# Kernel tuning notes

Measured on AMD Instinct MI355X. Metric: run time of the kernel, lower is better.

The kernel has to match this reference:

```python
import jax, jax.numpy as jnp
import numpy as np

N_NODES = 100000
N_EDGES = 3200000
IN_DIM = 3
HID = 8
OUT_DIM = 1


def setup_inputs() -> dict:
    key = jax.random.key(0)
    ks = jax.random.split(key, 10)
    x = jax.random.normal(ks[0], (N_NODES, IN_DIM), dtype=jnp.float32)
    edge_index = jax.random.randint(ks[1], (2, N_EDGES), 0, N_NODES, dtype=jnp.int64)
    cat_dim = 2 * (HID + IN_DIM)  # 22
    s = lambda fan_in: 1.0 / np.sqrt(fan_in)
    W_in = jax.random.uniform(ks[2], (IN_DIM, HID), jnp.float32, -s(IN_DIM), s(IN_DIM))
    b_in = jnp.zeros((HID,), jnp.float32)
    W1 = jax.random.uniform(ks[3], (cat_dim, HID), jnp.float32, -s(cat_dim), s(cat_dim))
    b1 = jnp.zeros((HID,), jnp.float32)
    W2 = jax.random.uniform(ks[4], (HID, HID), jnp.float32, -s(HID), s(HID))
    b2 = jnp.zeros((HID,), jnp.float32)
    W_e = jax.random.uniform(ks[5], (cat_dim, OUT_DIM), jnp.float32, -s(cat_dim), s(cat_dim))
    b_e = jnp.zeros((OUT_DIM,), jnp.float32)
    return {"x": x, "edge_index": edge_index, "W_in": W_in, "b_in": b_in,
            "W1": W1, "b1": b1, "W2": W2, "b2": b2, "W_e": W_e, "b_e": b_e}


def reference(x, edge_index, W_in, b_in, W1, b1, W2, b2, W_e, b_e):
    src = edge_index[0]  # j (source)
    dst = edge_index[1]  # i (target)

    # inputnet: Linear + Tanh
    H = jnp.tanh(x @ W_in + b_in)               # [N, HID]
    feat = jnp.concatenate([H, x], axis=-1)      # [N, HID+IN_DIM]

    # One EdgeConv iteration (n_iters=1): message = nn(cat([x_i, x_j - x_i]))
    xi = feat[dst]                                # [E, 11]
    xj = feat[src]                                # [E, 11]
    e = jnp.concatenate([xi, xj - xi], axis=-1)   # [E, 22]
    m = jax.nn.sigmoid(e @ W1 + b1)               # [E, HID]
    m = jax.nn.sigmoid(m @ W2 + b2)               # [E, HID]
    H = jax.ops.segment_sum(m, dst, num_segments=N_NODES)  # scatter-add to targets
    feat = jnp.concatenate([H, x], axis=-1)       # [N, 11]

    # edgenetwork on concatenated endpoint features
    ef = jnp.concatenate([feat[src], feat[dst]], axis=-1)   # [E, 22]
    out = jax.nn.sigmoid(ef @ W_e + b_e)          # [E, 1]
    return out.squeeze(-1)                        # [E]
```

## Files before the change

kernel.cpp:

```cpp
#include <hip/hip_runtime.h>
#include <hip/hip_fp16.h>

#define TPB     256
#define BSH     9
#define BW      512
#define EPB     8192
#define NBMAX   256
#define S_SPLIT 16
#define FXS     2097152.0f
#define FXSI    (1.0f / 2097152.0f)

static __device__ __forceinline__ float sigmoidf(float v) {
    return __builtin_amdgcn_rcpf(1.0f + __expf(-v));
}

static __device__ __forceinline__ void unpack8(uint4 u, float o[8]) {
    union { unsigned int u; __half2 h; } c0, c1, c2, c3;
    c0.u = u.x; c1.u = u.y; c2.u = u.z; c3.u = u.w;
    float2 f0 = __half22float2(c0.h), f1 = __half22float2(c1.h);
    float2 f2 = __half22float2(c2.h), f3 = __half22float2(c3.h);
    o[0]=f0.x; o[1]=f0.y; o[2]=f1.x; o[3]=f1.y;
    o[4]=f2.x; o[5]=f2.y; o[6]=f3.x; o[7]=f3.y;
}

__global__ void k_prep(const float* __restrict__ x,
                       const float* __restrict__ W_in,
                       const float* __restrict__ b_in,
                       const float* __restrict__ W1,
                       const float* __restrict__ b1,
                       float* __restrict__ egi,
                       __half* __restrict__ egjh,
                       const int* __restrict__ dst,
                       int* __restrict__ raw,
                       int n_nodes, int n_edges, int NB, int NBLK) {
    __shared__ int cnt[NBMAX];
    int t = threadIdx.x;
    if ((int)blockIdx.x < NBLK) {
        for (int b = t; b < NB; b += TPB) cnt[b] = 0;
        __syncthreads();
        int e0 = blockIdx.x * EPB;
#pragma unroll
        for (int k = 0; k < EPB / (TPB * 4); ++k) {
            int e = e0 + k * TPB * 4 + t * 4;
            if (e + 3 < n_edges) {
                int4 d4 = *(const int4*)(dst + e);
                atomicAdd(&cnt[d4.x >> BSH], 1);
                atomicAdd(&cnt[d4.y >> BSH], 1);
                atomicAdd(&cnt[d4.z >> BSH], 1);
                atomicAdd(&cnt[d4.w >> BSH], 1);
            } else {
                int qe = min(e + 4, n_edges);
                for (int q = e; q < qe; ++q)
                    atomicAdd(&cnt[dst[q] >> BSH], 1);
            }
        }
        __syncthreads();
        for (int b = t; b < NB; b += TPB)
            raw[(size_t)blockIdx.x * NB + b] = cnt[b];
    } else {
        int n = ((int)blockIdx.x - NBLK) * TPB + t;
        if (n >= n_nodes) return;
        float x0 = x[3*n], x1 = x[3*n+1], x2 = x[3*n+2];
        float f[11];
#pragma unroll
        for (int c = 0; c < 8; ++c)
            f[c] = tanhf(b_in[c] + x0*W_in[c] + x1*W_in[8+c] + x2*W_in[16+c]);
        f[8] = x0; f[9] = x1; f[10] = x2;
        float giv[8], gjv[8];
#pragma unroll
        for (int h = 0; h < 8; ++h) {
            float vi = b1[h], vj = 0.0f;
#pragma unroll
            for (int k = 0; k < 11; ++k) {
                float wa = W1[k*8+h], wb = W1[(11+k)*8+h];
                vi += f[k] * (wa - wb);
                vj += f[k] * wb;
            }
            giv[h] = __expf(-vi); gjv[h] = __expf(-vj);
        }
        float4* gip = (float4*)(egi + (size_t)n * 8);
        gip[0] = make_float4(giv[0], giv[1], giv[2], giv[3]);
        gip[1] = make_float4(giv[4], giv[5], giv[6], giv[7]);
        __align__(16) __half hj[8];
#pragma unroll
        for (int k = 0; k < 8; ++k) hj[k] = __float2half_rn(gjv[k]);
        *(uint4*)(egjh + (size_t)n * 8) = *(const uint4*)hj;
    }
}

__global__ void k_scan_cols(const int* __restrict__ raw, int* __restrict__ rel,
                            int* __restrict__ totals, int NB, int NBLK) {
    __shared__ int s[TPB];
    int b = blockIdx.x, t = threadIdx.x;
    int carry = 0;
    for (int q = 0; q < NBLK; q += TPB) {
        int blk = q + t;
        int v = (blk < NBLK) ? raw[(size_t)blk * NB + b] : 0;
        __syncthreads();
        s[t] = v; __syncthreads();
        for (int o = 1; o < TPB; o <<= 1) {
            int u = (t >= o) ? s[t - o] : 0;
            __syncthreads();
            s[t] += u;
            __syncthreads();
        }
        if (blk < NBLK) rel[(size_t)blk * NB + b] = carry + s[t] - v;
        carry += s[TPB - 1];
    }
    if (t == 0) totals[b] = carry;
}

__global__ void k_base(const int* __restrict__ totals, int* __restrict__ base,
                       int NB) {
    __shared__ int s[NBMAX];
    int t = threadIdx.x;
    int v = (t < NB) ? ((totals[t] + 3) & ~3) : 0;
    s[t] = v; __syncthreads();
    for (int o = 1; o < NBMAX; o <<= 1) {
        int u = (t >= o) ? s[t - o] : 0;
        __syncthreads();
        s[t] += u;
        __syncthreads();
    }
    if (t < NB) base[t] = s[t] - v;
}

__launch_bounds__(TPB)
__global__ void k_scatter(const int* __restrict__ src, const int* __restrict__ dst,
                          const int* __restrict__ raw, const int* __restrict__ rel,
                          const int* __restrict__ base,
                          int* __restrict__ sorted, int n_edges, int NB) {
    __shared__ int stage[EPB];
    __shared__ int cnt[NBMAX];
    __shared__ int lscan[NBMAX];
    __shared__ int gd[NBMAX];
    __shared__ int s[TPB];
    int t = threadIdx.x;

    {
        int v = (t < NB) ? raw[(size_t)blockIdx.x * NB + t] : 0;
        s[t] = v; __syncthreads();
        for (int o = 1; o < TPB; o <<= 1) {
            int u = (t >= o) ? s[t - o] : 0;
            __syncthreads();
            s[t] += u;
            __syncthreads();
        }
        if (t < NB) {
            lscan[t] = s[t] - v;
            cnt[t]   = s[t] - v;
            gd[t]    = base[t] + rel[(size_t)blockIdx.x * NB + t];
        }
    }
    __syncthreads();

    int e0 = blockIdx.x * EPB;
#pragma unroll
    for (int k = 0; k < EPB / (TPB * 4); ++k) {
        int e = e0 + k * TPB * 4 + t * 4;
        if (e + 3 < n_edges) {
            int4 s4 = *(const int4*)(src + e);
            int4 d4 = *(const int4*)(dst + e);
            int p;
            p = atomicAdd(&cnt[d4.x >> BSH], 1); stage[p] = (s4.x << BSH) | (d4.x & (BW-1));
            p = atomicAdd(&cnt[d4.y >> BSH], 1); stage[p] = (s4.y << BSH) | (d4.y & (BW-1));
            p = atomicAdd(&cnt[d4.z >> BSH], 1); stage[p] = (s4.z << BSH) | (d4.z & (BW-1));
            p = atomicAdd(&cnt[d4.w >> BSH], 1); stage[p] = (s4.w << BSH) | (d4.w & (BW-1));
        } else {
            int qe = min(e + 4, n_edges);
            for (int q = e; q < qe; ++q) {
                int d = dst[q];
                int p = atomicAdd(&cnt[d >> BSH], 1);
                stage[p] = (src[q] << BSH) | (d & (BW - 1));
            }
        }
    }
    __syncthreads();

    int wid = t >> 6, lane = t & 63;
    for (int b = wid; b < NB; b += (TPB / 64)) {
        int ls = lscan[b];
        int le = cnt[b];
        int g0 = gd[b];
        for (int i = ls + lane; i < le; i += 64)
            sorted[g0 + (i - ls)] = stage[i];
    }
}

__launch_bounds__(TPB, 4)
__global__ void k_bucket(const int* __restrict__ sorted, const int* __restrict__ base,
                         const int* __restrict__ totals,
                         const float* __restrict__ egi, const __half* __restrict__ egjh,
                         const float* __restrict__ W2, const float* __restrict__ b2,
                         const float* __restrict__ W_e,
                         int* __restrict__ part, int n_nodes, int NB, int NBP) {
    __shared__ int sa[BW], sc[BW];
    int t = threadIdx.x;
    int sl = blockIdx.x / NBP;
    int b  = blockIdx.x - sl * NBP;
    if (b >= NB) return;

    int nb0 = b * BW;
    for (int i = t; i < BW; i += TPB) { sa[i] = 0; sc[i] = 0; }
    __syncthreads();

    int beg = base[b];
    int len = totals[b];
    int qs = (((len + S_SPLIT - 1) / S_SPLIT) + 3) & ~3;
    int s0 = beg + sl * qs;
    int s1 = min(beg + len, s0 + qs);

    for (int g = s0 + t * 4; g < s1; g += TPB * 4) {
        if (g + 4 <= s1) {
            int4 pp = *(const int4*)(sorted + g);
            int d[4]  = { pp.x & (BW-1), pp.y & (BW-1), pp.z & (BW-1), pp.w & (BW-1) };
            int sj[4] = { pp.x >> BSH,   pp.y >> BSH,   pp.z >> BSH,   pp.w >> BSH };
            float ej[4][8];
#pragma unroll
            for (int q = 0; q < 4; ++q)
                unpack8(*(const uint4*)(egjh + (size_t)sj[q] * 8), ej[q]);
            float m[4][8];
#pragma unroll
            for (int q = 0; q < 4; ++q) {
                const float4* ip = (const float4*)(egi + (size_t)(nb0 + d[q]) * 8);
                float4 A = ip[0], B = ip[1];
                float ei[8] = {A.x,A.y,A.z,A.w,B.x,B.y,B.z,B.w};
#pragma unroll
                for (int k = 0; k < 8; ++k)
                    m[q][k] = __builtin_amdgcn_rcpf(1.0f + ei[k] * ej[q][k]);
            }
            float pa[4] = {0,0,0,0}, pc[4] = {0,0,0,0};
#pragma unroll
            for (int h = 0; h < 8; ++h) {
                float bb = b2[h];
                float v[4] = {bb, bb, bb, bb};
#pragma unroll
                for (int k = 0; k < 8; ++k) {
                    float w = W2[k*8+h];
#pragma unroll
                    for (int q = 0; q < 4; ++q) v[q] += m[q][k] * w;
                }
                float wa = W_e[h], wc = W_e[11+h];
#pragma unroll
                for (int q = 0; q < 4; ++q) {
                    float z = sigmoidf(v[q]);
                    pa[q] += z * wa; pc[q] += z * wc;
                }
            }
#pragma unroll
            for (int q = 0; q < 4; ++q) {
                atomicAdd(&sa[d[q]], __float2int_rn(pa[q] * FXS));
                atomicAdd(&sc[d[q]], __float2int_rn(pc[q] * FXS));
            }
        } else {
            for (int e = g; e < s1; ++e) {
                int p = sorted[e];
                int dl = p & (BW - 1);
                float ej[8];
                unpack8(*(const uint4*)(egjh + (size_t)(p >> BSH) * 8), ej);
                const float4* ip = (const float4*)(egi + (size_t)(nb0 + dl) * 8);
                float4 A = ip[0], B = ip[1];
                float ei[8] = {A.x,A.y,A.z,A.w,B.x,B.y,B.z,B.w};
                float m[8];
#pragma unroll
                for (int k = 0; k < 8; ++k)
                    m[k] = __builtin_amdgcn_rcpf(1.0f + ei[k] * ej[k]);
                float pa = 0, pc = 0;
#pragma unroll
                for (int h = 0; h < 8; ++h) {
                    float v = b2[h];
#pragma unroll
                    for (int k = 0; k < 8; ++k) v += m[k] * W2[k*8+h];
                    float z = sigmoidf(v);
                    pa += z * W_e[h]; pc += z * W_e[11+h];
                }
                atomicAdd(&sa[dl], __float2int_rn(pa * FXS));
                atomicAdd(&sc[dl], __float2int_rn(pc * FXS));
            }
        }
    }
    __syncthreads();
    size_t row = (size_t)blockIdx.x * (2 * BW);
    for (int i = t; i < BW; i += TPB) {
        part[row + i]      = sa[i];
        part[row + BW + i] = sc[i];
    }
}

__global__ void k_acc(const int* __restrict__ part, const float* __restrict__ x,
                      const float* __restrict__ W_e, float* __restrict__ ac,
                      int n_nodes, int NBP) {
    int n = blockIdx.x * blockDim.x + threadIdx.x;
    if (n >= n_nodes) return;
    int b = n >> BSH, r = n & (BW - 1);
    int ia = 0, ic = 0;
#pragma unroll
    for (int s = 0; s < S_SPLIT; ++s) {
        const int* pp = part + ((size_t)(s * NBP + b)) * (2 * BW);
        ia += pp[r];
        ic += pp[BW + r];
    }
    float a = (float)ia * FXSI, c = (float)ic * FXSI;
    float x0 = x[3*n], x1 = x[3*n+1], x2 = x[3*n+2];
    a += x0 * W_e[8]  + x1 * W_e[9]  + x2 * W_e[10];
    c += x0 * W_e[19] + x1 * W_e[20] + x2 * W_e[21];
    ac[2*n]     = a;
    ac[2*n + 1] = c;
}

__global__ void k_out2(const int* __restrict__ src, const int* __restrict__ dst,
                       const float* __restrict__ ac, const float* __restrict__ b_e,
                       float* __restrict__ out, int n_edges) {
    float bb = b_e[0];
    int e = (blockIdx.x * blockDim.x + threadIdx.x) * 4;
    if (e + 3 < n_edges) {
        int4 s4 = *(const int4*)(src + e);
        int4 d4 = *(const int4*)(dst + e);
        float4 o;
        o.x = sigmoidf(ac[2*s4.x] + ac[2*d4.x + 1] + bb);
        o.y = sigmoidf(ac[2*s4.y] + ac[2*d4.y + 1] + bb);
        o.z = sigmoidf(ac[2*s4.z] + ac[2*d4.z + 1] + bb);
        o.w = sigmoidf(ac[2*s4.w] + ac[2*d4.w + 1] + bb);
        *(float4*)(out + e) = o;
    } else {
        for (int q = e; q < n_edges; ++q)
            out[q] = sigmoidf(ac[2*src[q]] + ac[2*dst[q] + 1] + bb);
    }
}

__global__ void k_nodes(const float* __restrict__ x, const float* __restrict__ W_in,
                        const float* __restrict__ b_in, float* __restrict__ feat,
                        float* __restrict__ H2, int n_nodes) {
    int i = blockIdx.x * blockDim.x + threadIdx.x;
    if (i >= n_nodes) return;
    float x0 = x[3*i], x1 = x[3*i+1], x2 = x[3*i+2];
    float h[8];
#pragma unroll
    for (int c = 0; c < 8; ++c)
        h[c] = tanhf(b_in[c] + x0*W_in[c] + x1*W_in[8+c] + x2*W_in[16+c]);
    float4* fp = (float4*)(feat + (size_t)i * 12);
    fp[0] = make_float4(h[0],h[1],h[2],h[3]);
    fp[1] = make_float4(h[4],h[5],h[6],h[7]);
    fp[2] = make_float4(x0,x1,x2,0.0f);
    float4* hp = (float4*)(H2 + (size_t)i * 8);
    hp[0] = make_float4(0,0,0,0); hp[1] = make_float4(0,0,0,0);
}

__global__ void k_edges(const int* __restrict__ src, const int* __restrict__ dst,
                        const float* __restrict__ feat, const float* __restrict__ W1,
                        const float* __restrict__ b1, const float* __restrict__ W2,
                        const float* __restrict__ b2, float* __restrict__ H2,
                        int n_edges) {
    __shared__ float sW1[176], sW2[64], sb1[8], sb2[8];
    for (int t = threadIdx.x; t < 176; t += blockDim.x) sW1[t] = W1[t];
    for (int t = threadIdx.x; t < 64;  t += blockDim.x) sW2[t] = W2[t];
    if (threadIdx.x < 8) { sb1[threadIdx.x]=b1[threadIdx.x]; sb2[threadIdx.x]=b2[threadIdx.x]; }
    __syncthreads();
    int e = blockIdx.x * blockDim.x + threadIdx.x;
    if (e >= n_edges) return;
    int j = src[e], i = dst[e];
    const float4* fi = (const float4*)(feat + (size_t)i * 12);
    const float4* fj = (const float4*)(feat + (size_t)j * 12);
    float4 i0=fi[0],i1=fi[1],i2=fi[2],j0=fj[0],j1=fj[1],j2=fj[2];
    float xi[11]={i0.x,i0.y,i0.z,i0.w,i1.x,i1.y,i1.z,i1.w,i2.x,i2.y,i2.z};
    float xj[11]={j0.x,j0.y,j0.z,j0.w,j1.x,j1.y,j1.z,j1.w,j2.x,j2.y,j2.z};
    float dd[11];
#pragma unroll
    for (int k = 0; k < 11; ++k) dd[k]=xj[k]-xi[k];
    float m[8];
#pragma unroll
    for (int h = 0; h < 8; ++h) {
        float v = sb1[h];
#pragma unroll
        for (int k = 0; k < 11; ++k) v += xi[k]*sW1[k*8+h];
#pragma unroll
        for (int k = 0; k < 11; ++k) v += dd[k]*sW1[(11+k)*8+h];
        m[h] = sigmoidf(v);
    }
    float m2[8];
#pragma unroll
    for (int h = 0; h < 8; ++h) {
        float v = sb2[h];
#pragma unroll
        for (int k = 0; k < 8; ++k) v += m[k]*sW2[k*8+h];
        m2[h] = sigmoidf(v);
    }
    float* hp = H2 + (size_t)i * 8;
#pragma unroll
    for (int h = 0; h < 8; ++h) atomicAdd(hp + h, m2[h]);
}

__global__ void k_out(const int* __restrict__ src, const int* __restrict__ dst,
                      const float* __restrict__ H2, const float* __restrict__ x,
                      const float* __restrict__ W_e, const float* __restrict__ b_e,
                      float* __restrict__ out, int n_edges) {
    __shared__ float sW[22]; __shared__ float sb;
    if (threadIdx.x < 22) sW[threadIdx.x] = W_e[threadIdx.x];
    if (threadIdx.x == 0) sb = b_e[0];
    __syncthreads();
    int e = blockIdx.x * blockDim.x + threadIdx.x;
    if (e >= n_edges) return;
    int j = src[e], i = dst[e];
    const float4* hj = (const float4*)(H2 + (size_t)j * 8);
    const float4* hi = (const float4*)(H2 + (size_t)i * 8);
    float4 a0=hj[0],a1=hj[1],c0=hi[0],c1=hi[1];
    float acc = sb;
    acc += a0.x*sW[0]+a0.y*sW[1]+a0.z*sW[2]+a0.w*sW[3];
    acc += a1.x*sW[4]+a1.y*sW[5]+a1.z*sW[6]+a1.w*sW[7];
    acc += x[3*(size_t)j]*sW[8]+x[3*(size_t)j+1]*sW[9]+x[3*(size_t)j+2]*sW[10];
    acc += c0.x*sW[11]+c0.y*sW[12]+c0.z*sW[13]+c0.w*sW[14];
    acc += c1.x*sW[15]+c1.y*sW[16]+c1.z*sW[17]+c1.w*sW[18];
    acc += x[3*(size_t)i]*sW[19]+x[3*(size_t)i+1]*sW[20]+x[3*(size_t)i+2]*sW[21];
    out[e] = sigmoidf(acc);
}

extern "C" void kernel_launch(void* const* d_in, const int* in_sizes, int n_in,
                              void* d_out, int out_size, void* d_ws, size_t ws_size,
                              hipStream_t stream) {
    const float* x    = (const float*)d_in[0];
    const int*   ei   = (const int*)d_in[1];
    const float* W_in = (const float*)d_in[2];
    const float* b_in = (const float*)d_in[3];
    const float* W1   = (const float*)d_in[4];
    const float* b1   = (const float*)d_in[5];
    const float* W2   = (const float*)d_in[6];
    const float* b2   = (const float*)d_in[7];
    const float* W_e  = (const float*)d_in[8];
    const float* b_e  = (const float*)d_in[9];

    const int n_nodes = in_sizes[0] / 3;
    const int n_edges = in_sizes[1] / 2;
    const int* src = ei;
    const int* dst = ei + n_edges;
    float* out = (float*)d_out;

    const int NB   = (n_nodes + BW - 1) >> BSH;
    const int NBP  = (NB + 7) & ~7;
    const int NBLK = (n_edges + EPB - 1) / EPB;
    const int NFB  = (n_nodes + TPB - 1) / TPB;

    size_t off = 0;
    auto carve = [&](size_t bytes) { size_t o = off; off += (bytes + 255) & ~(size_t)255; return o; };
    char* ws = (char*)d_ws;
    size_t o_egi    = carve((size_t)n_nodes * 8 * 4);
    size_t o_egjh   = carve((size_t)n_nodes * 8 * 2);
    size_t o_ac     = carve((size_t)n_nodes * 2 * 4);
    size_t o_raw    = carve((size_t)NBLK * NB * 4);
    size_t o_rel    = carve((size_t)NBLK * NB * 4);
    size_t o_totals = carve((size_t)NB * 4);
    size_t o_base   = carve(((size_t)NB + 1) * 4);
    size_t o_sorted = carve(((size_t)n_edges + 4 * NBMAX) * 4);
    size_t o_part   = carve((size_t)NBP * S_SPLIT * 2 * BW * 4);
    bool fast = (off <= ws_size) && (NB <= NBMAX);

    if (fast) {
        float*  egi    = (float*)(ws + o_egi);
        __half* egjh   = (__half*)(ws + o_egjh);
        float*  ac     = (float*)(ws + o_ac);
        int*    raw    = (int*)(ws + o_raw);
        int*    rel    = (int*)(ws + o_rel);
        int*    totals = (int*)(ws + o_totals);
        int*    base   = (int*)(ws + o_base);
        int*    sorted = (int*)(ws + o_sorted);
        int*    part   = (int*)(ws + o_part);

        k_prep     <<<NBLK + NFB, TPB, 0, stream>>>(x, W_in, b_in, W1, b1, egi, egjh,
                                                    dst, raw, n_nodes, n_edges, NB, NBLK);
        k_scan_cols<<<NB, TPB, 0, stream>>>(raw, rel, totals, NB, NBLK);
        k_base     <<<1, NBMAX, 0, stream>>>(totals, base, NB);
        k_scatter  <<<NBLK, TPB, 0, stream>>>(src, dst, raw, rel, base, sorted, n_edges, NB);
        k_bucket   <<<NBP * S_SPLIT, TPB, 0, stream>>>(sorted, base, totals, egi, egjh, W2, b2, W_e,
                                                       part, n_nodes, NB, NBP);
        k_acc      <<<(n_nodes + TPB - 1) / TPB, TPB, 0, stream>>>(part, x, W_e, ac, n_nodes, NBP);
        k_out2     <<<(n_edges / 4 + TPB - 1) / TPB + 1, TPB, 0, stream>>>(src, dst, ac, b_e, out, n_edges);
    } else {
        float* feat = (float*)d_ws;
        float* H2   = feat + (size_t)n_nodes * 12;
        k_nodes<<<(n_nodes + TPB - 1) / TPB, TPB, 0, stream>>>(x, W_in, b_in, feat, H2, n_nodes);
        k_edges<<<(n_edges + TPB - 1) / TPB, TPB, 0, stream>>>(src, dst, feat, W1, b1, W2, b2, H2, n_edges);
        k_out  <<<(n_edges + TPB - 1) / TPB, TPB, 0, stream>>>(src, dst, H2, x, W_e, b_e, out, n_edges);
    }
}
```

Measured before the change: 100.00 us.

## Prefetch next edge batch gathers and halve slice split

The edge-message loop is restructured into a software pipeline. Each iteration issues the packed-index load and the four half-precision source-feature gathers for the next batch before it computes on the current one, to hide gather latency. The number of slices per node block is halved, giving fewer blocks with longer loops and fewer partial rows to reduce later. The trade-off is more live registers, which may lower occupancy, and less parallelism from the smaller grid.

```diff
diff --git a/kernel.cpp b/kernel.cpp
--- a/kernel.cpp
+++ b/kernel.cpp
@@ -6,7 +6,7 @@
 #define BW      512
 #define EPB     8192
 #define NBMAX   256
-#define S_SPLIT 16
+#define S_SPLIT 8
 #define FXS     2097152.0f
 #define FXSI    (1.0f / 2097152.0f)
 
@@ -210,73 +210,93 @@
     int s0 = beg + sl * qs;
     int s1 = min(beg + len, s0 + qs);
 
-    for (int g = s0 + t * 4; g < s1; g += TPB * 4) {
-        if (g + 4 <= s1) {
-            int4 pp = *(const int4*)(sorted + g);
-            int d[4]  = { pp.x & (BW-1), pp.y & (BW-1), pp.z & (BW-1), pp.w & (BW-1) };
-            int sj[4] = { pp.x >> BSH,   pp.y >> BSH,   pp.z >> BSH,   pp.w >> BSH };
-            float ej[4][8];
-#pragma unroll
-            for (int q = 0; q < 4; ++q)
-                unpack8(*(const uint4*)(egjh + (size_t)sj[q] * 8), ej[q]);
-            float m[4][8];
+    int g = s0 + t * 4;
+    bool v4 = (g + 4 <= s1);
+    int4 pp = make_int4(0,0,0,0);
+    uint4 uj[4];
+    if (v4) {
+        pp = *(const int4*)(sorted + g);
+        uj[0] = *(const uint4*)(egjh + (size_t)(pp.x >> BSH) * 8);
+        uj[1] = *(const uint4*)(egjh + (size_t)(pp.y >> BSH) * 8);
+        uj[2] = *(const uint4*)(egjh + (size_t)(pp.z >> BSH) * 8);
+        uj[3] = *(const uint4*)(egjh + (size_t)(pp.w >> BSH) * 8);
+    }
+    while (v4) {
+        int g2 = g + TPB * 4;
+        bool v4n = (g2 + 4 <= s1);
+        int4 pp2 = pp;
+        uint4 uj2[4] = { uj[0], uj[1], uj[2], uj[3] };
+        if (v4n) {
+            pp2 = *(const int4*)(sorted + g2);
+            uj2[0] = *(const uint4*)(egjh + (size_t)(pp2.x >> BSH) * 8);
+            uj2[1] = *(const uint4*)(egjh + (size_t)(pp2.y >> BSH) * 8);
+            uj2[2] = *(const uint4*)(egjh + (size_t)(pp2.z >> BSH) * 8);
+            uj2[3] = *(const uint4*)(egjh + (size_t)(pp2.w >> BSH) * 8);
+        }
+        int d[4] = { pp.x & (BW-1), pp.y & (BW-1), pp.z & (BW-1), pp.w & (BW-1) };
+        float ej[4][8];
+        unpack8(uj[0], ej[0]); unpack8(uj[1], ej[1]);
+        unpack8(uj[2], ej[2]); unpack8(uj[3], ej[3]);
+        float m[4][8];
+#pragma unroll
+        for (int q = 0; q < 4; ++q) {
+            const float4* ip = (const float4*)(egi + (size_t)(nb0 + d[q]) * 8);
+            float4 A = ip[0], B = ip[1];
+            float ei[8] = {A.x,A.y,A.z,A.w,B.x,B.y,B.z,B.w};
+#pragma unroll
+            for (int k = 0; k < 8; ++k)
+                m[q][k] = __builtin_amdgcn_rcpf(1.0f + ei[k] * ej[q][k]);
+        }
+        float pa[4] = {0,0,0,0}, pc[4] = {0,0,0,0};
+#pragma unroll
+        for (int h = 0; h < 8; ++h) {
+            float bb = b2[h];
+            float v[4] = {bb, bb, bb, bb};
+#pragma unroll
+            for (int k = 0; k < 8; ++k) {
+                float w = W2[k*8+h];
+#pragma unroll
+                for (int q = 0; q < 4; ++q) v[q] += m[q][k] * w;
+            }
+            float wa = W_e[h], wc = W_e[11+h];
 #pragma unroll
             for (int q = 0; q < 4; ++q) {
-                const float4* ip = (const float4*)(egi + (size_t)(nb0 + d[q]) * 8);
-                float4 A = ip[0], B = ip[1];
-                float ei[8] = {A.x,A.y,A.z,A.w,B.x,B.y,B.z,B.w};
-#pragma unroll
-                for (int k = 0; k < 8; ++k)
-                    m[q][k] = __builtin_amdgcn_rcpf(1.0f + ei[k] * ej[q][k]);
+                float z = sigmoidf(v[q]);
+                pa[q] += z * wa; pc[q] += z * wc;
             }
-            float pa[4] = {0,0,0,0}, pc[4] = {0,0,0,0};
+        }
+#pragma unroll
+        for (int q = 0; q < 4; ++q) {
+            atomicAdd(&sa[d[q]], __float2int_rn(pa[q] * FXS));
+            atomicAdd(&sc[d[q]], __float2int_rn(pc[q] * FXS));
+        }
+        pp = pp2; uj[0] = uj2[0]; uj[1] = uj2[1]; uj[2] = uj2[2]; uj[3] = uj2[3];
+        g = g2; v4 = v4n;
+    }
+    if (g < s1) {
+        for (int e = g; e < s1; ++e) {
+            int p = sorted[e];
+            int dl = p & (BW - 1);
+            float ej[8];
+            unpack8(*(const uint4*)(egjh + (size_t)(p >> BSH) * 8), ej);
+            const float4* ip = (const float4*)(egi + (size_t)(nb0 + dl) * 8);
+            float4 A = ip[0], B = ip[1];
+            float ei[8] = {A.x,A.y,A.z,A.w,B.x,B.y,B.z,B.w};
+            float m[8];
+#pragma unroll
+            for (int k = 0; k < 8; ++k)
+                m[k] = __builtin_amdgcn_rcpf(1.0f + ei[k] * ej[k]);
+            float pa = 0, pc = 0;
 #pragma unroll
             for (int h = 0; h < 8; ++h) {
-                float bb = b2[h];
-                float v[4] = {bb, bb, bb, bb};
-#pragma unroll
-                for (int k = 0; k < 8; ++k) {
-                    float w = W2[k*8+h];
-#pragma unroll
-                    for (int q = 0; q < 4; ++q) v[q] += m[q][k] * w;
-                }
-                float wa = W_e[h], wc = W_e[11+h];
-#pragma unroll
-                for (int q = 0; q < 4; ++q) {
-                    float z = sigmoidf(v[q]);
-                    pa[q] += z * wa; pc[q] += z * wc;
-                }
+                float v = b2[h];
+#pragma unroll
+                for (int k = 0; k < 8; ++k) v += m[k] * W2[k*8+h];
+                float z = sigmoidf(v);
+                pa += z * W_e[h]; pc += z * W_e[11+h];
             }
-#pragma unroll
-            for (int q = 0; q < 4; ++q) {
-                atomicAdd(&sa[d[q]], __float2int_rn(pa[q] * FXS));
-                atomicAdd(&sc[d[q]], __float2int_rn(pc[q] * FXS));
-            }
-        } else {
-            for (int e = g; e < s1; ++e) {
-                int p = sorted[e];
-                int dl = p & (BW - 1);
-                float ej[8];
-                unpack8(*(const uint4*)(egjh + (size_t)(p >> BSH) * 8), ej);
-                const float4* ip = (const float4*)(egi + (size_t)(nb0 + dl) * 8);
-                float4 A = ip[0], B = ip[1];
-                float ei[8] = {A.x,A.y,A.z,A.w,B.x,B.y,B.z,B.w};
-                float m[8];
-#pragma unroll
-                for (int k = 0; k < 8; ++k)
-                    m[k] = __builtin_amdgcn_rcpf(1.0f + ei[k] * ej[k]);
-                float pa = 0, pc = 0;
-#pragma unroll
-                for (int h = 0; h < 8; ++h) {
-                    float v = b2[h];
-#pragma unroll
-                    for (int k = 0; k < 8; ++k) v += m[k] * W2[k*8+h];
-                    float z = sigmoidf(v);
-                    pa += z * W_e[h]; pc += z * W_e[11+h];
-                }
-                atomicAdd(&sa[dl], __float2int_rn(pa * FXS));
-                atomicAdd(&sc[dl], __float2int_rn(pc * FXS));
-            }
+            atomicAdd(&sa[dl], __float2int_rn(pa * FXS));
+            atomicAdd(&sc[dl], __float2int_rn(pc * FXS));
         }
     }
     __syncthreads();
```

New measurement: 101.3 us. Within noise of the previous version (+1.3%).

## Replace global histogram-scan bucketing with atomic per-bucket cursors into fixed slots

Applied to the files above, without the earlier changes.

Removes the separate dst histogram pass, the per-bucket column scan and the base scan kernels. Each scatter block now counts its own edges per bucket, then reserves space in a fixed-capacity slot with one global atomicAdd per bucket. k_bucket derives each bucket's start and length from the slot index and the final cursor. This cuts two kernel launches and the extra read of dst. In exchange, the order of edges within a bucket becomes nondeterministic, and correctness relies on no bucket exceeding its slot (average plus 8192), which holds for near-uniform destinations but is unchecked.

```diff
diff --git a/kernel.cpp b/kernel.cpp
--- a/kernel.cpp
+++ b/kernel.cpp
@@ -30,105 +30,45 @@
                        const float* __restrict__ b1,
                        float* __restrict__ egi,
                        __half* __restrict__ egjh,
-                       const int* __restrict__ dst,
-                       int* __restrict__ raw,
-                       int n_nodes, int n_edges, int NB, int NBLK) {
-    __shared__ int cnt[NBMAX];
+                       int* __restrict__ cursor,
+                       int n_nodes, int NB, int SLOT, int NFB) {
     int t = threadIdx.x;
-    if ((int)blockIdx.x < NBLK) {
-        for (int b = t; b < NB; b += TPB) cnt[b] = 0;
-        __syncthreads();
-        int e0 = blockIdx.x * EPB;
-#pragma unroll
-        for (int k = 0; k < EPB / (TPB * 4); ++k) {
-            int e = e0 + k * TPB * 4 + t * 4;
-            if (e + 3 < n_edges) {
-                int4 d4 = *(const int4*)(dst + e);
-                atomicAdd(&cnt[d4.x >> BSH], 1);
-                atomicAdd(&cnt[d4.y >> BSH], 1);
-                atomicAdd(&cnt[d4.z >> BSH], 1);
-                atomicAdd(&cnt[d4.w >> BSH], 1);
-            } else {
-                int qe = min(e + 4, n_edges);
-                for (int q = e; q < qe; ++q)
-                    atomicAdd(&cnt[dst[q] >> BSH], 1);
-            }
+    if ((int)blockIdx.x == NFB) {
+        if (t < NB) cursor[t] = t * SLOT;
+        return;
+    }
+    int n = blockIdx.x * TPB + t;
+    if (n >= n_nodes) return;
+    float x0 = x[3*n], x1 = x[3*n+1], x2 = x[3*n+2];
+    float f[11];
+#pragma unroll
+    for (int c = 0; c < 8; ++c)
+        f[c] = tanhf(b_in[c] + x0*W_in[c] + x1*W_in[8+c] + x2*W_in[16+c]);
+    f[8] = x0; f[9] = x1; f[10] = x2;
+    float giv[8], gjv[8];
+#pragma unroll
+    for (int h = 0; h < 8; ++h) {
+        float vi = b1[h], vj = 0.0f;
+#pragma unroll
+        for (int k = 0; k < 11; ++k) {
+            float wa = W1[k*8+h], wb = W1[(11+k)*8+h];
+            vi += f[k] * (wa - wb);
+            vj += f[k] * wb;
         }
-        __syncthreads();
-        for (int b = t; b < NB; b += TPB)
-            raw[(size_t)blockIdx.x * NB + b] = cnt[b];
-    } else {
-        int n = ((int)blockIdx.x - NBLK) * TPB + t;
-        if (n >= n_nodes) return;
-        float x0 = x[3*n], x1 = x[3*n+1], x2 = x[3*n+2];
-        float f[11];
-#pragma unroll
-        for (int c = 0; c < 8; ++c)
-            f[c] = tanhf(b_in[c] + x0*W_in[c] + x1*W_in[8+c] + x2*W_in[16+c]);
-        f[8] = x0; f[9] = x1; f[10] = x2;
-        float giv[8], gjv[8];
-#pragma unroll
-        for (int h = 0; h < 8; ++h) {
-            float vi = b1[h], vj = 0.0f;
-#pragma unroll
-            for (int k = 0; k < 11; ++k) {
-                float wa = W1[k*8+h], wb = W1[(11+k)*8+h];
-                vi += f[k] * (wa - wb);
-                vj += f[k] * wb;
-            }
-            giv[h] = __expf(-vi); gjv[h] = __expf(-vj);
-        }
-        float4* gip = (float4*)(egi + (size_t)n * 8);
-        gip[0] = make_float4(giv[0], giv[1], giv[2], giv[3]);
-        gip[1] = make_float4(giv[4], giv[5], giv[6], giv[7]);
-        __align__(16) __half hj[8];
-#pragma unroll
-        for (int k = 0; k < 8; ++k) hj[k] = __float2half_rn(gjv[k]);
-        *(uint4*)(egjh + (size_t)n * 8) = *(const uint4*)hj;
-    }
-}
-
-__global__ void k_scan_cols(const int* __restrict__ raw, int* __restrict__ rel,
-                            int* __restrict__ totals, int NB, int NBLK) {
-    __shared__ int s[TPB];
-    int b = blockIdx.x, t = threadIdx.x;
-    int carry = 0;
-    for (int q = 0; q < NBLK; q += TPB) {
-        int blk = q + t;
-        int v = (blk < NBLK) ? raw[(size_t)blk * NB + b] : 0;
-        __syncthreads();
-        s[t] = v; __syncthreads();
-        for (int o = 1; o < TPB; o <<= 1) {
-            int u = (t >= o) ? s[t - o] : 0;
-            __syncthreads();
-            s[t] += u;
-            __syncthreads();
-        }
-        if (blk < NBLK) rel[(size_t)blk * NB + b] = carry + s[t] - v;
-        carry += s[TPB - 1];
-    }
-    if (t == 0) totals[b] = carry;
-}
-
-__global__ void k_base(const int* __restrict__ totals, int* __restrict__ base,
-                       int NB) {
-    __shared__ int s[NBMAX];
-    int t = threadIdx.x;
-    int v = (t < NB) ? ((totals[t] + 3) & ~3) : 0;
-    s[t] = v; __syncthreads();
-    for (int o = 1; o < NBMAX; o <<= 1) {
-        int u = (t >= o) ? s[t - o] : 0;
-        __syncthreads();
-        s[t] += u;
-        __syncthreads();
-    }
-    if (t < NB) base[t] = s[t] - v;
+        giv[h] = __expf(-vi); gjv[h] = __expf(-vj);
+    }
+    float4* gip = (float4*)(egi + (size_t)n * 8);
+    gip[0] = make_float4(giv[0], giv[1], giv[2], giv[3]);
+    gip[1] = make_float4(giv[4], giv[5], giv[6], giv[7]);
+    __align__(16) __half hj[8];
+#pragma unroll
+    for (int k = 0; k < 8; ++k) hj[k] = __float2half_rn(gjv[k]);
+    *(uint4*)(egjh + (size_t)n * 8) = *(const uint4*)hj;
 }
 
 __launch_bounds__(TPB)
 __global__ void k_scatter(const int* __restrict__ src, const int* __restrict__ dst,
-                          const int* __restrict__ raw, const int* __restrict__ rel,
-                          const int* __restrict__ base,
+                          int* __restrict__ cursor,
                           int* __restrict__ sorted, int n_edges, int NB) {
     __shared__ int stage[EPB];
     __shared__ int cnt[NBMAX];
@@ -136,25 +76,42 @@
     __shared__ int gd[NBMAX];
     __shared__ int s[TPB];
     int t = threadIdx.x;
-
-    {
-        int v = (t < NB) ? raw[(size_t)blockIdx.x * NB + t] : 0;
-        s[t] = v; __syncthreads();
-        for (int o = 1; o < TPB; o <<= 1) {
-            int u = (t >= o) ? s[t - o] : 0;
-            __syncthreads();
-            s[t] += u;
-            __syncthreads();
+    for (int b = t; b < NB; b += TPB) cnt[b] = 0;
+    __syncthreads();
+
+    int e0 = blockIdx.x * EPB;
+#pragma unroll
+    for (int k = 0; k < EPB / (TPB * 4); ++k) {
+        int e = e0 + k * TPB * 4 + t * 4;
+        if (e + 3 < n_edges) {
+            int4 d4 = *(const int4*)(dst + e);
+            atomicAdd(&cnt[d4.x >> BSH], 1);
+            atomicAdd(&cnt[d4.y >> BSH], 1);
+            atomicAdd(&cnt[d4.z >> BSH], 1);
+            atomicAdd(&cnt[d4.w >> BSH], 1);
+        } else {
+            int qe = min(e + 4, n_edges);
+            for (int q = e; q < qe; ++q)
+                atomicAdd(&cnt[dst[q] >> BSH], 1);
         }
-        if (t < NB) {
-            lscan[t] = s[t] - v;
-            cnt[t]   = s[t] - v;
-            gd[t]    = base[t] + rel[(size_t)blockIdx.x * NB + t];
-        }
-    }
-    __syncthreads();
-
-    int e0 = blockIdx.x * EPB;
+    }
+    __syncthreads();
+
+    int v = (t < NB) ? cnt[t] : 0;
+    s[t] = v; __syncthreads();
+    for (int o = 1; o < TPB; o <<= 1) {
+        int u = (t >= o) ? s[t - o] : 0;
+        __syncthreads();
+        s[t] += u;
+        __syncthreads();
+    }
+    if (t < NB) {
+        lscan[t] = s[t] - v;
+        cnt[t]   = s[t] - v;
+        gd[t]    = atomicAdd(&cursor[t], v);
+    }
+    __syncthreads();
+
 #pragma unroll
     for (int k = 0; k < EPB / (TPB * 4); ++k) {
         int e = e0 + k * TPB * 4 + t * 4;
@@ -188,12 +145,11 @@
 }
 
 __launch_bounds__(TPB, 4)
-__global__ void k_bucket(const int* __restrict__ sorted, const int* __restrict__ base,
-                         const int* __restrict__ totals,
+__global__ void k_bucket(const int* __restrict__ sorted, const int* __restrict__ cursor,
                          const float* __restrict__ egi, const __half* __restrict__ egjh,
                          const float* __restrict__ W2, const float* __restrict__ b2,
                          const float* __restrict__ W_e,
-                         int* __restrict__ part, int n_nodes, int NB, int NBP) {
+                         int* __restrict__ part, int n_nodes, int NB, int NBP, int SLOT) {
     __shared__ int sa[BW], sc[BW];
     int t = threadIdx.x;
     int sl = blockIdx.x / NBP;
@@ -204,8 +160,8 @@
     for (int i = t; i < BW; i += TPB) { sa[i] = 0; sc[i] = 0; }
     __syncthreads();
 
-    int beg = base[b];
-    int len = totals[b];
+    int beg = b * SLOT;
+    int len = cursor[b] - beg;
     int qs = (((len + S_SPLIT - 1) / S_SPLIT) + 3) & ~3;
     int s0 = beg + sl * qs;
     int s1 = min(beg + len, s0 + qs);
@@ -438,6 +394,7 @@
     const int NBP  = (NB + 7) & ~7;
     const int NBLK = (n_edges + EPB - 1) / EPB;
     const int NFB  = (n_nodes + TPB - 1) / TPB;
+    const int SLOT = (((n_edges + NB - 1) / NB) + 8192 + 3) & ~3;
 
     size_t off = 0;
     auto carve = [&](size_t bytes) { size_t o = off; off += (bytes + 255) & ~(size_t)255; return o; };
@@ -445,11 +402,8 @@
     size_t o_egi    = carve((size_t)n_nodes * 8 * 4);
     size_t o_egjh   = carve((size_t)n_nodes * 8 * 2);
     size_t o_ac     = carve((size_t)n_nodes * 2 * 4);
-    size_t o_raw    = carve((size_t)NBLK * NB * 4);
-    size_t o_rel    = carve((size_t)NBLK * NB * 4);
-    size_t o_totals = carve((size_t)NB * 4);
-    size_t o_base   = carve(((size_t)NB + 1) * 4);
-    size_t o_sorted = carve(((size_t)n_edges + 4 * NBMAX) * 4);
+    size_t o_cursor = carve((size_t)NB * 4);
+    size_t o_sorted = carve((size_t)NB * SLOT * 4 + 16);
     size_t o_part   = carve((size_t)NBP * S_SPLIT * 2 * BW * 4);
     bool fast = (off <= ws_size) && (NB <= NBMAX);
 
@@ -457,22 +411,17 @@
         float*  egi    = (float*)(ws + o_egi);
         __half* egjh   = (__half*)(ws + o_egjh);
         float*  ac     = (float*)(ws + o_ac);
-        int*    raw    = (int*)(ws + o_raw);
-        int*    rel    = (int*)(ws + o_rel);
-        int*    totals = (int*)(ws + o_totals);
-        int*    base   = (int*)(ws + o_base);
+        int*    cursor = (int*)(ws + o_cursor);
         int*    sorted = (int*)(ws + o_sorted);
         int*    part   = (int*)(ws + o_part);
 
-        k_prep     <<<NBLK + NFB, TPB, 0, stream>>>(x, W_in, b_in, W1, b1, egi, egjh,
-                                                    dst, raw, n_nodes, n_edges, NB, NBLK);
-        k_scan_cols<<<NB, TPB, 0, stream>>>(raw, rel, totals, NB, NBLK);
-        k_base     <<<1, NBMAX, 0, stream>>>(totals, base, NB);
-        k_scatter  <<<NBLK, TPB, 0, stream>>>(src, dst, raw, rel, base, sorted, n_edges, NB);
-        k_bucket   <<<NBP * S_SPLIT, TPB, 0, stream>>>(sorted, base, totals, egi, egjh, W2, b2, W_e,
-                                                       part, n_nodes, NB, NBP);
-        k_acc      <<<(n_nodes + TPB - 1) / TPB, TPB, 0, stream>>>(part, x, W_e, ac, n_nodes, NBP);
-        k_out2     <<<(n_edges / 4 + TPB - 1) / TPB + 1, TPB, 0, stream>>>(src, dst, ac, b_e, out, n_edges);
+        k_prep   <<<NFB + 1, TPB, 0, stream>>>(x, W_in, b_in, W1, b1, egi, egjh,
+                                               cursor, n_nodes, NB, SLOT, NFB);
+        k_scatter<<<NBLK, TPB, 0, stream>>>(src, dst, cursor, sorted, n_edges, NB);
+        k_bucket <<<NBP * S_SPLIT, TPB, 0, stream>>>(sorted, cursor, egi, egjh, W2, b2, W_e,
+                                                     part, n_nodes, NB, NBP, SLOT);
+        k_acc    <<<(n_nodes + TPB - 1) / TPB, TPB, 0, stream>>>(part, x, W_e, ac, n_nodes, NBP);
+        k_out2   <<<(n_edges / 4 + TPB - 1) / TPB + 1, TPB, 0, stream>>>(src, dst, ac, b_e, out, n_edges);
     } else {
         float* feat = (float*)d_ws;
         float* H2   = feat + (size_t)n_nodes * 12;
```

After: 101.7 us. No clear change (+1.7%).
